# Kernel optimization log

Hardware: AMD Instinct MI355X
Metric: run time of the kernel (lower is better)

The kernel has to match this reference:

```python
import jax, jax.numpy as jnp
import numpy as np

N_NODES = 50000


def sage_conv(x, src, dst, Wl, bl, Wr):
    # PyG SAGEConv (aggr='mean'): out = lin_l(mean_j x_j) + lin_r(x_i)
    msg = x[src]                                            # [E, d] gather
    agg = jax.ops.segment_sum(msg, dst, num_segments=N_NODES)   # [N, d]
    cnt = jax.ops.segment_sum(jnp.ones_like(dst, dtype=x.dtype), dst,
                              num_segments=N_NODES)         # [N]
    agg = agg / jnp.maximum(cnt, 1.0)[:, None]
    return agg @ Wl.T + bl + x @ Wr.T


def setup_inputs() -> dict:
    key = jax.random.key(0)
    ks = jax.random.split(key, 8)
    d = 64
    x = jax.random.normal(ks[0], (N_NODES, d), dtype=jnp.float32)
    edge_index = jax.random.randint(ks[1], (2, 800000), 0, N_NODES, dtype=jnp.int64)
    s = 1.0 / np.sqrt(d)
    Wl0 = jax.random.uniform(ks[2], (d, d), jnp.float32, -s, s)
    bl0 = jax.random.uniform(ks[3], (d,), jnp.float32, -s, s)
    Wr0 = jax.random.uniform(ks[4], (d, d), jnp.float32, -s, s)
    Wl1 = jax.random.uniform(ks[5], (d, d), jnp.float32, -s, s)
    bl1 = jax.random.uniform(ks[6], (d,), jnp.float32, -s, s)
    Wr1 = jax.random.uniform(ks[7], (d, d), jnp.float32, -s, s)
    return {"x": x, "edge_index": edge_index,
            "Wl0": Wl0, "bl0": bl0, "Wr0": Wr0,
            "Wl1": Wl1, "bl1": bl1, "Wr1": Wr1}


def reference(x, edge_index, Wl0, bl0, Wr0, Wl1, bl1, Wr1):
    src, dst = edge_index[0], edge_index[1]
    h = sage_conv(x, src, dst, Wl0, bl0, Wr0)
    h = jax.nn.relu(h)
    h = sage_conv(h, src, dst, Wl1, bl1, Wr1)
    return h
```

## Files before the change

kernel.cpp:

```cpp
#include <hip/hip_runtime.h>

#define N_NODES 50000
#define D 64
#define BKT_SHIFT 10
#define BKT_NODES 1024
#define NBKT ((N_NODES + BKT_NODES - 1) / BKT_NODES)
#define CAP 18432
#define GPAD 32
#define XBLOCKS ((N_NODES * D / 4) / 256)

typedef __attribute__((ext_vector_type(4))) float f4;
typedef __attribute__((ext_vector_type(4))) unsigned uv4;
typedef __attribute__((ext_vector_type(4))) unsigned short us4;
typedef __attribute__((ext_vector_type(8))) short bf16x8;
typedef __attribute__((ext_vector_type(4))) float f32x4;

static __device__ __forceinline__ unsigned short f2bf(float f) {
    unsigned u = __builtin_bit_cast(unsigned, f);
    unsigned r = (u + 0x7fffu + ((u >> 16) & 1u)) >> 16;
    return (unsigned short)r;
}
static __device__ __forceinline__ float bflo(unsigned w) {
    return __builtin_bit_cast(float, w << 16);
}
static __device__ __forceinline__ float bfhi(unsigned w) {
    return __builtin_bit_cast(float, w & 0xffff0000u);
}

static __device__ __forceinline__ int detect_is64(const unsigned* __restrict__ ei32) {
    int lane = threadIdx.x & 63;
    unsigned v = (lane < 32) ? ei32[2 * lane + 1] : 0u;
    return (__ballot(v != 0u) == 0ull) ? 1 : 0;
}

static __device__ __forceinline__ int load_edges4(const unsigned* __restrict__ ei32,
                                                  int is64, int E, int base,
                                                  int* s, int* d) {
    if (base + 3 < E) {
        if (is64) {
            uv4 sa = *(const uv4*)&ei32[2 * base];
            uv4 sb = *(const uv4*)&ei32[2 * base + 4];
            uv4 da = *(const uv4*)&ei32[2 * (E + base)];
            uv4 db = *(const uv4*)&ei32[2 * (E + base) + 4];
            s[0] = (int)sa[0]; s[1] = (int)sa[2]; s[2] = (int)sb[0]; s[3] = (int)sb[2];
            d[0] = (int)da[0]; d[1] = (int)da[2]; d[2] = (int)db[0]; d[3] = (int)db[2];
        } else {
            uv4 sa = *(const uv4*)&ei32[base];
            uv4 da = *(const uv4*)&ei32[E + base];
            s[0] = (int)sa[0]; s[1] = (int)sa[1]; s[2] = (int)sa[2]; s[3] = (int)sa[3];
            d[0] = (int)da[0]; d[1] = (int)da[1]; d[2] = (int)da[2]; d[3] = (int)da[3];
        }
        return 4;
    }
    int c = 0;
    for (int e = base; e < E && e < base + 4; ++e, ++c) {
        s[c] = is64 ? (int)ei32[2 * e] : (int)ei32[e];
        d[c] = is64 ? (int)ei32[2 * (E + e)] : (int)ei32[E + e];
    }
    return c;
}

__global__ __launch_bounds__(256) void cvt_all(const float* __restrict__ x,
                                               unsigned short* __restrict__ xb,
                                               const float* __restrict__ Wl0,
                                               const float* __restrict__ Wr0,
                                               const float* __restrict__ Wl1,
                                               const float* __restrict__ Wr1,
                                               unsigned short* __restrict__ Wlb0,
                                               unsigned short* __restrict__ Wrb0,
                                               unsigned short* __restrict__ Wlb1,
                                               unsigned short* __restrict__ Wrb1,
                                               int* __restrict__ gcur) {
    int b = blockIdx.x, tid = threadIdx.x;
    if (b < XBLOCKS) {
        int i = (b * 256 + tid) * 4;
        f4 v = *(const f4*)&x[i];
        us4 o;
        o[0] = f2bf(v[0]); o[1] = f2bf(v[1]); o[2] = f2bf(v[2]); o[3] = f2bf(v[3]);
        *(us4*)&xb[i] = o;
    } else if (b < XBLOCKS + 4) {
        int w = b - XBLOCKS;
        const float* src = (w == 0) ? Wl0 : (w == 1) ? Wr0 : (w == 2) ? Wl1 : Wr1;
        unsigned short* dst = (w == 0) ? Wlb0 : (w == 1) ? Wrb0 : (w == 2) ? Wlb1 : Wrb1;
        for (int i = tid * 4; i < 64 * 64; i += 1024) {
            f4 v = *(const f4*)&src[i];
            us4 o;
            o[0] = f2bf(v[0]); o[1] = f2bf(v[1]); o[2] = f2bf(v[2]); o[3] = f2bf(v[3]);
            *(us4*)&dst[i] = o;
        }
    } else {
        if (tid < NBKT) gcur[tid * GPAD] = tid * CAP;
    }
}

__global__ __launch_bounds__(256) void bin_kernel(const unsigned* __restrict__ ei32,
                                                  int E, int* __restrict__ gcur,
                                                  unsigned* __restrict__ binned) {
    __shared__ int bc[NBKT];
    __shared__ int boff[NBKT];
    int tid = threadIdx.x;
    if (tid < NBKT) bc[tid] = 0;
    __syncthreads();
    int is64 = detect_is64(ei32);
    int base = (blockIdx.x * 256 + tid) * 8;
    int s[8], d[8];
    int c = 0;
    if (base < E) {
        c = load_edges4(ei32, is64, E, base, s, d);
        if (base + 4 < E) c += load_edges4(ei32, is64, E, base + 4, s + 4, d + 4);
    }
    for (int t = 0; t < c; ++t) atomicAdd(&bc[d[t] >> BKT_SHIFT], 1);
    __syncthreads();
    if (tid < NBKT) {
        int v = bc[tid];
        boff[tid] = v ? atomicAdd(&gcur[tid * GPAD], v) : 0;
        bc[tid] = 0;
    }
    __syncthreads();
    for (int t = 0; t < c; ++t) {
        int bkt = d[t] >> BKT_SHIFT;
        int pos = boff[bkt] + atomicAdd(&bc[bkt], 1);
        if (pos < (bkt + 1) * CAP)
            binned[pos] = ((unsigned)(d[t] & (BKT_NODES - 1)) << 16) | (unsigned)s[t];
    }
}

__global__ __launch_bounds__(1024) void build_kernel(const unsigned* __restrict__ binned,
                                                     const int* __restrict__ gcur,
                                                     int2* __restrict__ rp2,
                                                     unsigned short* __restrict__ ssrc, int n) {
    __shared__ int nc[BKT_NODES];
    __shared__ int wpart[16];
    int b = blockIdx.x;
    int tid = threadIdx.x;
    int ebase = b * CAP;
    int eend = gcur[b * GPAD];
    if (eend > ebase + CAP) eend = ebase + CAP;
    nc[tid] = 0;
    __syncthreads();
    for (int i = ebase + tid; i < eend; i += 1024)
        atomicAdd(&nc[binned[i] >> 16], 1);
    __syncthreads();
    int v = nc[tid];
    int lane = tid & 63, wv = tid >> 6;
    int incl = v;
#pragma unroll
    for (int off = 1; off < 64; off <<= 1) {
        int t = __shfl_up(incl, off);
        if (lane >= off) incl += t;
    }
    if (lane == 63) wpart[wv] = incl;
    __syncthreads();
    int pre = 0;
    for (int w2 = 0; w2 < wv; ++w2) pre += wpart[w2];
    int run = ebase + pre + incl - v;
    int node = b * BKT_NODES + tid;
    nc[tid] = run;
    if (node < n) rp2[node] = make_int2(run, v);
    __syncthreads();
    for (int i = ebase + tid; i < eend; i += 1024) {
        unsigned u = binned[i];
        int pos = atomicAdd(&nc[u >> 16], 1);
        ssrc[pos] = (unsigned short)(u & 0xffffu);
    }
}

template <bool RELU, bool LAST>
__global__ __launch_bounds__(256) void sage_fused(const unsigned short* __restrict__ xb,
                                                  const int2* __restrict__ rp2,
                                                  const unsigned short* __restrict__ ssrc,
                                                  const unsigned short* __restrict__ Wlb,
                                                  const float* __restrict__ bl,
                                                  const unsigned short* __restrict__ Wrb,
                                                  float* __restrict__ out,
                                                  unsigned short* __restrict__ ob, int n) {
    int gw = (blockIdx.x * 256 + threadIdx.x) >> 6;
    int nb = gw * 16;
    if (nb >= n) return;
    int lane = threadIdx.x & 63;
    int row = lane & 15;
    int half = lane >> 4;
    int koff = half * 8;
    int node = nb + row;
    int2 bd = rp2[node];
    int beg = bd.x, end = bd.x + bd.y;

    float acc[16];
#pragma unroll
    for (int j = 0; j < 16; ++j) acc[j] = 0.f;

    int e = beg;
    for (; e + 1 < end; e += 2) {
        int s0 = ssrc[e], s1 = ssrc[e + 1];
        uv4 v0 = *(const uv4*)(xb + (size_t)s0 * 64 + koff);
        uv4 v1 = *(const uv4*)(xb + (size_t)s0 * 64 + 32 + koff);
        uv4 v2 = *(const uv4*)(xb + (size_t)s1 * 64 + koff);
        uv4 v3 = *(const uv4*)(xb + (size_t)s1 * 64 + 32 + koff);
#pragma unroll
        for (int q = 0; q < 4; ++q) {
            acc[2 * q]     += bflo(v0[q]) + bflo(v2[q]);
            acc[2 * q + 1] += bfhi(v0[q]) + bfhi(v2[q]);
            acc[8 + 2 * q]     += bflo(v1[q]) + bflo(v3[q]);
            acc[8 + 2 * q + 1] += bfhi(v1[q]) + bfhi(v3[q]);
        }
    }
    if (e < end) {
        int s0 = ssrc[e];
        uv4 v0 = *(const uv4*)(xb + (size_t)s0 * 64 + koff);
        uv4 v1 = *(const uv4*)(xb + (size_t)s0 * 64 + 32 + koff);
#pragma unroll
        for (int q = 0; q < 4; ++q) {
            acc[2 * q]     += bflo(v0[q]);
            acc[2 * q + 1] += bfhi(v0[q]);
            acc[8 + 2 * q]     += bflo(v1[q]);
            acc[8 + 2 * q + 1] += bfhi(v1[q]);
        }
    }

    float inv = 1.0f / (float)(bd.y > 1 ? bd.y : 1);
    uv4 pa0, pa1;
#pragma unroll
    for (int q = 0; q < 4; ++q) {
        pa0[q] = (unsigned)f2bf(acc[2 * q] * inv) |
                 ((unsigned)f2bf(acc[2 * q + 1] * inv) << 16);
        pa1[q] = (unsigned)f2bf(acc[8 + 2 * q] * inv) |
                 ((unsigned)f2bf(acc[8 + 2 * q + 1] * inv) << 16);
    }
    bf16x8 a0 = __builtin_bit_cast(bf16x8, pa0);
    bf16x8 a1 = __builtin_bit_cast(bf16x8, pa1);
    bf16x8 x0 = *(const bf16x8*)&xb[(size_t)node * 64 + koff];
    bf16x8 x1 = *(const bf16x8*)&xb[(size_t)node * 64 + 32 + koff];

    f32x4 accd[4];
#pragma unroll
    for (int ot = 0; ot < 4; ++ot) {
        int o = ot * 16 + row;
        float bv = bl[o];
        accd[ot] = (f32x4){bv, bv, bv, bv};
        bf16x8 wl0 = *(const bf16x8*)&Wlb[(size_t)o * 64 + koff];
        bf16x8 wl1 = *(const bf16x8*)&Wlb[(size_t)o * 64 + 32 + koff];
        bf16x8 wr0 = *(const bf16x8*)&Wrb[(size_t)o * 64 + koff];
        bf16x8 wr1 = *(const bf16x8*)&Wrb[(size_t)o * 64 + 32 + koff];
        accd[ot] = __builtin_amdgcn_mfma_f32_16x16x32_bf16(a0, wl0, accd[ot], 0, 0, 0);
        accd[ot] = __builtin_amdgcn_mfma_f32_16x16x32_bf16(a1, wl1, accd[ot], 0, 0, 0);
        accd[ot] = __builtin_amdgcn_mfma_f32_16x16x32_bf16(x0, wr0, accd[ot], 0, 0, 0);
        accd[ot] = __builtin_amdgcn_mfma_f32_16x16x32_bf16(x1, wr1, accd[ot], 0, 0, 0);
    }
#pragma unroll
    for (int ot = 0; ot < 4; ++ot) {
        int o = ot * 16 + row;
#pragma unroll
        for (int r = 0; r < 4; ++r) {
            float v = accd[ot][r];
            if (RELU) v = fmaxf(v, 0.f);
            int nd = nb + half * 4 + r;
            if (LAST) out[(size_t)nd * 64 + o] = v;
            else      ob[(size_t)nd * 64 + o] = f2bf(v);
        }
    }
}

extern "C" void kernel_launch(void* const* d_in, const int* in_sizes, int n_in,
                              void* d_out, int out_size, void* d_ws, size_t ws_size,
                              hipStream_t stream) {
    const float* x      = (const float*)d_in[0];
    const unsigned* ei  = (const unsigned*)d_in[1];
    const float* Wl0    = (const float*)d_in[2];
    const float* bl0    = (const float*)d_in[3];
    const float* Wr0    = (const float*)d_in[4];
    const float* Wl1    = (const float*)d_in[5];
    const float* bl1    = (const float*)d_in[6];
    const float* Wr1    = (const float*)d_in[7];
    float* out          = (float*)d_out;

    const int N = N_NODES;
    const int E = in_sizes[1] / 2;

    char* w = (char*)d_ws;
    auto take = [&](size_t bytes) {
        char* p = w;
        w += (bytes + 255) & ~(size_t)255;
        return p;
    };
    int*            gcur   = (int*)take((size_t)NBKT * GPAD * sizeof(int));
    unsigned*       binned = (unsigned*)take((size_t)NBKT * CAP * sizeof(unsigned));
    int2*           rp2    = (int2*)take((size_t)N * sizeof(int2));
    unsigned short* ssrc   = (unsigned short*)take((size_t)NBKT * CAP * sizeof(unsigned short));
    unsigned short* xb     = (unsigned short*)take((size_t)N * D * sizeof(unsigned short));
    unsigned short* hb     = (unsigned short*)take((size_t)N * D * sizeof(unsigned short));
    unsigned short* Wlb0   = (unsigned short*)take((size_t)D * D * sizeof(unsigned short));
    unsigned short* Wrb0   = (unsigned short*)take((size_t)D * D * sizeof(unsigned short));
    unsigned short* Wlb1   = (unsigned short*)take((size_t)D * D * sizeof(unsigned short));
    unsigned short* Wrb1   = (unsigned short*)take((size_t)D * D * sizeof(unsigned short));

    cvt_all<<<XBLOCKS + 5, 256, 0, stream>>>(x, xb, Wl0, Wr0, Wl1, Wr1,
                                             Wlb0, Wrb0, Wlb1, Wrb1, gcur);
    int edgeBlocks = (E + 2047) / 2048;
    bin_kernel<<<edgeBlocks, 256, 0, stream>>>(ei, E, gcur, binned);
    build_kernel<<<NBKT, 1024, 0, stream>>>(binned, gcur, rp2, ssrc, N);

    int fusedBlocks = (N + 63) / 64;
    sage_fused<true, false><<<fusedBlocks, 256, 0, stream>>>(xb, rp2, ssrc, Wlb0, bl0, Wrb0,
                                                             nullptr, hb, N);
    sage_fused<false, true><<<fusedBlocks, 256, 0, stream>>>(hb, rp2, ssrc, Wlb1, bl1, Wrb1,
                                                             out, nullptr, N);
}
```

Measured before the change: 169.7 us.

## Split neighbor aggregation across four waves per 16-node tile with LDS reduction

Each block now handles 16 nodes instead of 64. Its four waves each gather a quarter of every node's edge list, and the partial sums are reduced through shared memory. Each wave then computes one 16-column output tile with MFMA instead of all four. This shortens each wave's serial gather chain, giving more memory-level parallelism and better load balance for the latency-bound gather. The cost is a block-wide barrier, an LDS round trip, and four times as many blocks, plus redundant reduction work in every wave.

```diff
diff --git a/kernel.cpp b/kernel.cpp
--- a/kernel.cpp
+++ b/kernel.cpp
@@ -174,20 +174,25 @@
                                                   const unsigned short* __restrict__ Wrb,
                                                   float* __restrict__ out,
                                                   unsigned short* __restrict__ ob, int n) {
-    int gw = (blockIdx.x * 256 + threadIdx.x) >> 6;
-    int nb = gw * 16;
-    if (nb >= n) return;
-    int lane = threadIdx.x & 63;
+    __shared__ f4 lred[4][4][64];
+    int tid = threadIdx.x;
+    int wv = tid >> 6;
+    int lane = tid & 63;
+    int nb = blockIdx.x * 16;
     int row = lane & 15;
     int half = lane >> 4;
     int koff = half * 8;
     int node = nb + row;
     int2 bd = rp2[node];
-    int beg = bd.x, end = bd.x + bd.y;
-
-    float acc[16];
-#pragma unroll
-    for (int j = 0; j < 16; ++j) acc[j] = 0.f;
+    int deg = bd.y;
+    int chunk = (deg + 3) >> 2;
+    int beg = bd.x + wv * chunk;
+    int end = bd.x + deg;
+    if (end > beg + chunk) end = beg + chunk;
+
+    f4 acc4[4];
+#pragma unroll
+    for (int q = 0; q < 4; ++q) acc4[q] = (f4){0.f, 0.f, 0.f, 0.f};
 
     int e = beg;
     for (; e + 1 < end; e += 2) {
@@ -197,11 +202,15 @@
         uv4 v2 = *(const uv4*)(xb + (size_t)s1 * 64 + koff);
         uv4 v3 = *(const uv4*)(xb + (size_t)s1 * 64 + 32 + koff);
 #pragma unroll
-        for (int q = 0; q < 4; ++q) {
-            acc[2 * q]     += bflo(v0[q]) + bflo(v2[q]);
-            acc[2 * q + 1] += bfhi(v0[q]) + bfhi(v2[q]);
-            acc[8 + 2 * q]     += bflo(v1[q]) + bflo(v3[q]);
-            acc[8 + 2 * q + 1] += bfhi(v1[q]) + bfhi(v3[q]);
+        for (int q = 0; q < 2; ++q) {
+            acc4[q][0] += bflo(v0[2 * q])     + bflo(v2[2 * q]);
+            acc4[q][1] += bfhi(v0[2 * q])     + bfhi(v2[2 * q]);
+            acc4[q][2] += bflo(v0[2 * q + 1]) + bflo(v2[2 * q + 1]);
+            acc4[q][3] += bfhi(v0[2 * q + 1]) + bfhi(v2[2 * q + 1]);
+            acc4[2 + q][0] += bflo(v1[2 * q])     + bflo(v3[2 * q]);
+            acc4[2 + q][1] += bfhi(v1[2 * q])     + bfhi(v3[2 * q]);
+            acc4[2 + q][2] += bflo(v1[2 * q + 1]) + bflo(v3[2 * q + 1]);
+            acc4[2 + q][3] += bfhi(v1[2 * q + 1]) + bfhi(v3[2 * q + 1]);
         }
     }
     if (e < end) {
@@ -209,54 +218,65 @@
         uv4 v0 = *(const uv4*)(xb + (size_t)s0 * 64 + koff);
         uv4 v1 = *(const uv4*)(xb + (size_t)s0 * 64 + 32 + koff);
 #pragma unroll
-        for (int q = 0; q < 4; ++q) {
-            acc[2 * q]     += bflo(v0[q]);
-            acc[2 * q + 1] += bfhi(v0[q]);
-            acc[8 + 2 * q]     += bflo(v1[q]);
-            acc[8 + 2 * q + 1] += bfhi(v1[q]);
+        for (int q = 0; q < 2; ++q) {
+            acc4[q][0] += bflo(v0[2 * q]);
+            acc4[q][1] += bfhi(v0[2 * q]);
+            acc4[q][2] += bflo(v0[2 * q + 1]);
+            acc4[q][3] += bfhi(v0[2 * q + 1]);
+            acc4[2 + q][0] += bflo(v1[2 * q]);
+            acc4[2 + q][1] += bfhi(v1[2 * q]);
+            acc4[2 + q][2] += bflo(v1[2 * q + 1]);
+            acc4[2 + q][3] += bfhi(v1[2 * q + 1]);
         }
     }
 
-    float inv = 1.0f / (float)(bd.y > 1 ? bd.y : 1);
+#pragma unroll
+    for (int q = 0; q < 4; ++q) lred[q][wv][lane] = acc4[q];
+    __syncthreads();
+#pragma unroll
+    for (int w2 = 0; w2 < 4; ++w2) {
+        if (w2 == wv) continue;
+#pragma unroll
+        for (int q = 0; q < 4; ++q) acc4[q] += lred[q][w2][lane];
+    }
+
+    float inv = 1.0f / (float)(deg > 1 ? deg : 1);
     uv4 pa0, pa1;
 #pragma unroll
-    for (int q = 0; q < 4; ++q) {
-        pa0[q] = (unsigned)f2bf(acc[2 * q] * inv) |
-                 ((unsigned)f2bf(acc[2 * q + 1] * inv) << 16);
-        pa1[q] = (unsigned)f2bf(acc[8 + 2 * q] * inv) |
-                 ((unsigned)f2bf(acc[8 + 2 * q + 1] * inv) << 16);
+    for (int q = 0; q < 2; ++q) {
+        pa0[2 * q]     = (unsigned)f2bf(acc4[q][0] * inv) |
+                         ((unsigned)f2bf(acc4[q][1] * inv) << 16);
+        pa0[2 * q + 1] = (unsigned)f2bf(acc4[q][2] * inv) |
+                         ((unsigned)f2bf(acc4[q][3] * inv) << 16);
+        pa1[2 * q]     = (unsigned)f2bf(acc4[2 + q][0] * inv) |
+                         ((unsigned)f2bf(acc4[2 + q][1] * inv) << 16);
+        pa1[2 * q + 1] = (unsigned)f2bf(acc4[2 + q][2] * inv) |
+                         ((unsigned)f2bf(acc4[2 + q][3] * inv) << 16);
     }
     bf16x8 a0 = __builtin_bit_cast(bf16x8, pa0);
     bf16x8 a1 = __builtin_bit_cast(bf16x8, pa1);
     bf16x8 x0 = *(const bf16x8*)&xb[(size_t)node * 64 + koff];
     bf16x8 x1 = *(const bf16x8*)&xb[(size_t)node * 64 + 32 + koff];
 
-    f32x4 accd[4];
-#pragma unroll
-    for (int ot = 0; ot < 4; ++ot) {
-        int o = ot * 16 + row;
-        float bv = bl[o];
-        accd[ot] = (f32x4){bv, bv, bv, bv};
-        bf16x8 wl0 = *(const bf16x8*)&Wlb[(size_t)o * 64 + koff];
-        bf16x8 wl1 = *(const bf16x8*)&Wlb[(size_t)o * 64 + 32 + koff];
-        bf16x8 wr0 = *(const bf16x8*)&Wrb[(size_t)o * 64 + koff];
-        bf16x8 wr1 = *(const bf16x8*)&Wrb[(size_t)o * 64 + 32 + koff];
-        accd[ot] = __builtin_amdgcn_mfma_f32_16x16x32_bf16(a0, wl0, accd[ot], 0, 0, 0);
-        accd[ot] = __builtin_amdgcn_mfma_f32_16x16x32_bf16(a1, wl1, accd[ot], 0, 0, 0);
-        accd[ot] = __builtin_amdgcn_mfma_f32_16x16x32_bf16(x0, wr0, accd[ot], 0, 0, 0);
-        accd[ot] = __builtin_amdgcn_mfma_f32_16x16x32_bf16(x1, wr1, accd[ot], 0, 0, 0);
-    }
-#pragma unroll
-    for (int ot = 0; ot < 4; ++ot) {
-        int o = ot * 16 + row;
-#pragma unroll
-        for (int r = 0; r < 4; ++r) {
-            float v = accd[ot][r];
-            if (RELU) v = fmaxf(v, 0.f);
-            int nd = nb + half * 4 + r;
-            if (LAST) out[(size_t)nd * 64 + o] = v;
-            else      ob[(size_t)nd * 64 + o] = f2bf(v);
-        }
+    int o = wv * 16 + row;
+    float bv = bl[o];
+    f32x4 accd = (f32x4){bv, bv, bv, bv};
+    bf16x8 wl0 = *(const bf16x8*)&Wlb[(size_t)o * 64 + koff];
+    bf16x8 wl1 = *(const bf16x8*)&Wlb[(size_t)o * 64 + 32 + koff];
+    bf16x8 wr0 = *(const bf16x8*)&Wrb[(size_t)o * 64 + koff];
+    bf16x8 wr1 = *(const bf16x8*)&Wrb[(size_t)o * 64 + 32 + koff];
+    accd = __builtin_amdgcn_mfma_f32_16x16x32_bf16(a0, wl0, accd, 0, 0, 0);
+    accd = __builtin_amdgcn_mfma_f32_16x16x32_bf16(a1, wl1, accd, 0, 0, 0);
+    accd = __builtin_amdgcn_mfma_f32_16x16x32_bf16(x0, wr0, accd, 0, 0, 0);
+    accd = __builtin_amdgcn_mfma_f32_16x16x32_bf16(x1, wr1, accd, 0, 0, 0);
+
+#pragma unroll
+    for (int r = 0; r < 4; ++r) {
+        float v = accd[r];
+        if (RELU) v = fmaxf(v, 0.f);
+        int nd = nb + half * 4 + r;
+        if (LAST) out[(size_t)nd * 64 + o] = v;
+        else      ob[(size_t)nd * 64 + o] = f2bf(v);
     }
 }
 
@@ -299,7 +319,7 @@
     bin_kernel<<<edgeBlocks, 256, 0, stream>>>(ei, E, gcur, binned);
     build_kernel<<<NBKT, 1024, 0, stream>>>(binned, gcur, rp2, ssrc, N);
 
-    int fusedBlocks = (N + 63) / 64;
+    int fusedBlocks = (N + 15) / 16;
     sage_fused<true, false><<<fusedBlocks, 256, 0, stream>>>(xb, rp2, ssrc, Wlb0, bl0, Wrb0,
                                                              nullptr, hb, N);
     sage_fused<false, true><<<fusedBlocks, 256, 0, stream>>>(hb, rp2, ssrc, Wlb1, bl1, Wrb1,
```

Result: faster. 164.5 us (-3.0%).
